# Optimization experiments

Measured on AMD Instinct MI355X. Metric: run time of the kernel, lower is better.

The kernel has to match this reference:

```python
import jax, jax.numpy as jnp
import numpy as np

# Dimensions
B_, T_, IN_ = 8, 1024, 512          # batch, seq_len, in_dim
D_ = 1024                           # latent_dim (hidden_size)
I_ = 2048                           # intermediate_size
N_ = 64                             # state_size
H_ = 16                             # ssm_num_head
P_ = I_ // H_                       # head_dim = 128
K_ = 3                              # conv_kernel
L_ = 4                              # num_layer
OUT_, CB_ = 512, 1024               # out_dim, num_code_book
CONV_DIM = I_ + 2 * N_              # 2176
PROJ = I_ + CONV_DIM + H_           # in_proj width of mixer = 4240


def setup_inputs() -> dict:
    key = jax.random.key(0)
    ks = jax.random.split(key, 16)
    s = 0.02
    inp = {
        "x": jax.random.normal(ks[0], (B_, T_, IN_), jnp.float32),
        "in_w": jax.random.normal(ks[1], (IN_, D_), jnp.float32) * s,
        "in_b": jnp.zeros((D_,), jnp.float32),
        "norm_w": jnp.ones((L_, D_), jnp.float32),
        "mix_in_w": jax.random.normal(ks[2], (L_, D_, PROJ), jnp.float32) * s,
        "conv_w": jax.random.normal(ks[3], (L_, K_, 1, CONV_DIM), jnp.float32) * s,
        "conv_b": jnp.zeros((L_, CONV_DIM), jnp.float32),
        "dt_bias": jax.random.normal(ks[4], (L_, H_), jnp.float32) * 0.1,
        "A_log": jnp.log(jax.random.uniform(ks[5], (L_, H_), jnp.float32, 0.001, 0.1)),
        "D": jnp.ones((L_, H_), jnp.float32),
        "gnorm_w": jnp.ones((L_, I_), jnp.float32),
        "mix_out_w": jax.random.normal(ks[6], (L_, I_, D_), jnp.float32) * s,
        "out_w": jax.random.normal(ks[7], (D_, OUT_), jnp.float32) * s,
        "out_b": jnp.zeros((OUT_,), jnp.float32),
        "code_w": jax.random.normal(ks[8], (D_, CB_), jnp.float32) * s,
        "code_b": jnp.zeros((CB_,), jnp.float32),
    }
    return inp


def rmsnorm(x, w, eps=1e-6):
    v = jnp.mean(jnp.square(x), axis=-1, keepdims=True)
    return x * jax.lax.rsqrt(v + eps) * w


def mamba_block(x, nw, inw, cw, cb, dtb, alog, Dv, gnw, outw):
    residual = x
    h = rmsnorm(x, nw)
    proj = h @ inw                                   # [B,T,PROJ]
    gate, hBC, dt = jnp.split(proj, [I_, I_ + CONV_DIM], axis=-1)
    # causal depthwise conv along time
    conv = jax.lax.conv_general_dilated(
        hBC, cw, window_strides=(1,), padding=[(K_ - 1, 0)],
        dimension_numbers=("NWC", "WIO", "NWC"), feature_group_count=CONV_DIM)
    conv = jax.nn.silu(conv + cb)
    xs, Bm, Cm = jnp.split(conv, [I_, I_ + N_], axis=-1)   # [B,T,I],[B,T,N],[B,T,N]
    dt = jax.nn.softplus(dt + dtb)                   # [B,T,H]
    a = -jnp.exp(alog)                               # [H] scalar decay per head
    xh = xs.reshape(B_, T_, H_, P_)

    def step(hst, inp):
        dt_t, B_t, C_t, x_t = inp                    # [B,H],[B,N],[B,N],[B,H,P]
        dA = jnp.exp(dt_t * a)                       # [B,H]
        hst = hst * dA[:, :, None, None] + (dt_t[:, :, None, None] * x_t[..., None]) * B_t[:, None, None, :]
        y = jnp.einsum("bhpn,bn->bhp", hst, C_t)
        return hst, y

    inputs = (dt.transpose(1, 0, 2), Bm.transpose(1, 0, 2),
              Cm.transpose(1, 0, 2), xh.transpose(1, 0, 2, 3))
    h0 = jnp.zeros((B_, H_, P_, N_), x.dtype)
    _, ys = jax.lax.scan(step, h0, inputs)           # ys: [T,B,H,P]
    y = ys.transpose(1, 0, 2, 3) + Dv[None, None, :, None] * xh
    y = y.reshape(B_, T_, I_)
    y = rmsnorm(y * jax.nn.silu(gate), gnw)          # gated RMSNorm
    return residual + y @ outw


def reference(x, in_w, in_b, norm_w, mix_in_w, conv_w, conv_b, dt_bias,
              A_log, D, gnorm_w, mix_out_w, out_w, out_b, code_w, code_b):
    h = x @ in_w + in_b
    for i in range(L_):
        h = mamba_block(h, norm_w[i], mix_in_w[i], conv_w[i], conv_b[i],
                        dt_bias[i], A_log[i], D[i], gnorm_w[i], mix_out_w[i])
    return (h @ out_w + out_b, h @ code_w + code_b)
```

## Files before the change

### kernel.cpp

```cpp
#include <hip/hip_runtime.h>
#include <hip/hip_bf16.h>

typedef __hip_bfloat16 bf16;
typedef __bf16 bfv8 __attribute__((ext_vector_type(8)));
typedef float fv4 __attribute__((ext_vector_type(4)));

#define B_  8
#define T_  1024
#define INP 512
#define D_  1024
#define I_  2048
#define N_  64
#define H_  16
#define P_  128
#define L_  4
#define OUT_ 512
#define CB_ 1024
#define CONV_DIM 2176
#define PROJ 4240
#define M_  (B_*T_)
#define TC  64
#define NC  (T_/TC)

typedef const __attribute__((address_space(1))) void gv_t;
typedef __attribute__((address_space(3))) void lv_t;

__device__ __forceinline__ void load_lds16(const bf16* g, char* l) {
    __builtin_amdgcn_global_load_lds((gv_t*)g, (lv_t*)l, 16, 0, 0);
}

template <int N> __device__ __forceinline__ void wait_vm() {
    if constexpr (N == 0)      asm volatile("s_waitcnt vmcnt(0)" ::: "memory");
    else if constexpr (N == 2) asm volatile("s_waitcnt vmcnt(2)" ::: "memory");
    else if constexpr (N == 3) asm volatile("s_waitcnt vmcnt(3)" ::: "memory");
    else if constexpr (N == 4) asm volatile("s_waitcnt vmcnt(4)" ::: "memory");
    else if constexpr (N == 6) asm volatile("s_waitcnt vmcnt(6)" ::: "memory");
    else                       asm volatile("s_waitcnt vmcnt(8)" ::: "memory");
}
__device__ __forceinline__ void barrier_sync() {
    asm volatile("s_barrier" ::: "memory");
}

__device__ __forceinline__ fv4 MF(bfv8 a, bfv8 b, fv4 c) {
    return __builtin_amdgcn_mfma_f32_16x16x32_bf16(a, b, c, 0, 0, 0);
}
__device__ __forceinline__ __bf16 f2b(float x) {
    __hip_bfloat16 h = __float2bfloat16(x);
    union { unsigned short u; __bf16 b; } t;
    t.u = *reinterpret_cast<unsigned short*>(&h);
    return t.b;
}
__device__ __forceinline__ float bb2f(__bf16 x) {
    union { __bf16 b; unsigned short u; } t; t.b = x;
    union { unsigned int u; float f; } r; r.u = (unsigned int)t.u << 16;
    return r.f;
}
__device__ __forceinline__ bfv8 cvt8f(const float* p) {
    float4 a = *(const float4*)p, b = *(const float4*)(p + 4);
    bfv8 r;
    r[0] = f2b(a.x); r[1] = f2b(a.y); r[2] = f2b(a.z); r[3] = f2b(a.w);
    r[4] = f2b(b.x); r[5] = f2b(b.y); r[6] = f2b(b.z); r[7] = f2b(b.w);
    return r;
}

__global__ __launch_bounds__(256) void ingest_k(const float* __restrict__ src,
                                                bf16* __restrict__ dst, int n) {
    int i = blockIdx.x * 256 + threadIdx.x;
    if (i >= n) return;
    dst[i] = __float2bfloat16(src[i]);
}

__global__ __launch_bounds__(256) void transpose_any(const float* __restrict__ in,
                                                     size_t off,
                                                     bf16* __restrict__ out,
                                                     int R, int C) {
    __shared__ bf16 tile[32][33];
    int c0 = blockIdx.x * 32, r0 = blockIdx.y * 32;
    int tx = threadIdx.x, ty = threadIdx.y;
#pragma unroll
    for (int i = 0; i < 4; ++i) {
        int r = r0 + ty + i * 8, c = c0 + tx;
        bf16 v = __float2bfloat16(0.f);
        if (c < C) v = __float2bfloat16(in[off + (size_t)r * C + c]);
        tile[ty + i * 8][tx] = v;
    }
    __syncthreads();
#pragma unroll
    for (int i = 0; i < 4; ++i) {
        int c = c0 + ty + i * 8;
        out[(size_t)c * R + r0 + tx] = tile[tx][ty + i * 8];
    }
}

template <int MODE, int BM, int BN, int WGM, int WGN, int RING, int NTHR>
__global__ __launch_bounds__(NTHR) void gemm8p(const bf16* __restrict__ A,
                                               const bf16* __restrict__ Bt,
                                               int K, int N,
                                               const bf16* __restrict__ bias,
                                               float* __restrict__ outF,
                                               bf16* __restrict__ outB,
                                               bf16* __restrict__ outB2,
                                               float* __restrict__ outF2) {
    constexpr int HK = 32;
    constexpr int MT = BM / WGM / 16;
    constexpr int NT = BN / WGN / 16;
    constexpr int ABY = BM * HK * 2;
    constexpr int BBY = BN * HK * 2;
    constexpr int BUF = ABY + BBY;
    constexpr int RPI = NTHR / 4;
    constexpr int AL = BM / RPI;
    constexpr int BL = BN / RPI;
    constexpr int LD = AL + BL;
    constexpr int IB = NTHR * 16;

    extern __shared__ char lds[];
    const int tid = threadIdx.x;
    const int wv = tid >> 6, lane = tid & 63;
    const int l16 = lane & 15, quad = lane >> 4;
    const int wm = (wv / WGN) * (BM / WGM);
    const int wn = (wv % WGN) * (BN / WGN);

    const int NX = gridDim.x;
    const int nwg = NX * gridDim.y;
    const int orig = blockIdx.y * NX + blockIdx.x;
    const int q = nwg >> 3, r = nwg & 7, xcd = orig & 7, lid = orig >> 3;
    const int wg = (xcd < r ? xcd * (q + 1) : r * (q + 1) + (xcd - r) * q) + lid;
    const int m0 = (wg / NX) * BM;
    const int n0 = (wg % NX) * BN;

    const int srow = tid >> 2, sslot = tid & 3;
    const int swz = (sslot ^ ((srow >> 1) & 3)) << 3;
    const bf16* ga = A  + (size_t)(m0 + srow) * K + swz;
    const bf16* gb = Bt + (size_t)(n0 + srow) * K + swz;
    char* lw = lds + wv * 1024;

    const int HT = K / HK;

    auto stageA = [&](int stg, int rbuf) {
#pragma unroll
        for (int j = 0; j < AL; ++j)
            load_lds16(ga + (size_t)stg * HK + (size_t)(j * RPI) * K,
                       lw + rbuf * BUF + j * IB);
    };
    auto stageB = [&](int stg, int rbuf) {
#pragma unroll
        for (int j = 0; j < BL; ++j)
            load_lds16(gb + (size_t)stg * HK + (size_t)(j * RPI) * K,
                       lw + rbuf * BUF + ABY + j * IB);
    };

#pragma unroll
    for (int h = 0; h < RING - 1; ++h) { stageA(h, h); stageB(h, h); }
    wait_vm<LD>();
    barrier_sync();

    fv4 acc[MT][NT] = {};
    int rb = 0;
    for (int ht = 0; ht < HT; ++ht) {
        const char* Ab = lds + rb * BUF;
        const char* Bb = Ab + ABY;
        const int stg = ht + RING - 1;
        const int sb = (rb == 0) ? RING - 1 : rb - 1;
        const bool dostage = stg < HT;

        bfv8 bf[NT], af[MT];
#pragma unroll
        for (int i = 0; i < NT; ++i) {
            int rr = wn + i * 16 + l16;
            bf[i] = *(const bfv8*)(Bb + rr * 64 + ((quad ^ ((rr >> 1) & 3)) << 4));
        }
#pragma unroll
        for (int i = 0; i < MT; ++i) {
            int rr = wm + i * 16 + l16;
            af[i] = *(const bfv8*)(Ab + rr * 64 + ((quad ^ ((rr >> 1) & 3)) << 4));
        }
        if (dostage) { stageA(stg, sb); stageB(stg, sb); }
        __builtin_amdgcn_s_setprio(1);
#pragma unroll
        for (int mt = 0; mt < MT; ++mt)
#pragma unroll
            for (int nt = 0; nt < NT; ++nt)
                acc[mt][nt] = MF(af[mt], bf[nt], acc[mt][nt]);
        __builtin_amdgcn_s_setprio(0);

        int fut = HT - 1 - ht; if (fut > RING - 1) fut = RING - 1;
        if (fut >= 1) {
            int w = (fut - 1) * LD;
            if (w >= LD) wait_vm<LD>();
            else wait_vm<0>();
        }
        barrier_sync();
        rb = (rb + 1 == RING) ? 0 : rb + 1;
    }

#pragma unroll
    for (int mt = 0; mt < MT; ++mt) {
#pragma unroll
        for (int nt = 0; nt < NT; ++nt) {
#pragma unroll
            for (int i = 0; i < 4; ++i) {
                int row = m0 + wm + mt * 16 + quad * 4 + i;
                int col = n0 + wn + nt * 16 + l16;
                float v = acc[mt][nt][i];
                if (MODE == 0) {
                    v += __bfloat162float(bias[col]);
                    outF[(size_t)row * N + col] = v;
                } else if (MODE == 1) {
                    if (col < I_)
                        outB[(size_t)row * I_ + col] = __float2bfloat16(v);
                    else if (col < I_ + CONV_DIM)
                        outB2[(size_t)row * CONV_DIM + (col - I_)] = __float2bfloat16(v);
                    else if (col < PROJ)
                        outF2[(size_t)row * H_ + (col - (I_ + CONV_DIM))] = v;
                } else if (MODE == 2) {
                    outF[(size_t)row * N + col] += v;
                }
            }
        }
    }
}

__global__ __launch_bounds__(256) void rmsnorm_k(const float* __restrict__ x,
                                                 const bf16* __restrict__ w,
                                                 bf16* __restrict__ out) {
    int row = blockIdx.x, tid = threadIdx.x;
    float4 v = *(const float4*)&x[(size_t)row * D_ + tid * 4];
    float ss = v.x * v.x + v.y * v.y + v.z * v.z + v.w * v.w;
#pragma unroll
    for (int off = 32; off; off >>= 1) ss += __shfl_down(ss, off);
    __shared__ float sb[4];
    if ((tid & 63) == 0) sb[tid >> 6] = ss;
    __syncthreads();
    ss = sb[0] + sb[1] + sb[2] + sb[3];
    float rs = rsqrtf(ss * (1.f / D_) + 1e-6f);
    float xv[4] = {v.x, v.y, v.z, v.w};
#pragma unroll
    for (int j = 0; j < 4; ++j)
        out[(size_t)row * D_ + tid * 4 + j] =
            __float2bfloat16(xv[j] * rs * __bfloat162float(w[tid * 4 + j]));
}

__global__ __launch_bounds__(256) void gatednorm_k(const bf16* __restrict__ y,
                                                   const bf16* __restrict__ g,
                                                   const bf16* __restrict__ w,
                                                   bf16* __restrict__ out) {
    int row = blockIdx.x, tid = threadIdx.x;
    size_t base = (size_t)row * I_ + tid * 8;
    bf16 yv[8], gv[8];
    *(uint4*)yv = *(const uint4*)&y[base];
    *(uint4*)gv = *(const uint4*)&g[base];
    float vv[8]; float ss = 0.f;
#pragma unroll
    for (int j = 0; j < 8; ++j) {
        float yf = __bfloat162float(yv[j]);
        float gf = __bfloat162float(gv[j]);
        float sig = 1.f / (1.f + expf(-gf));
        vv[j] = yf * gf * sig;
        ss += vv[j] * vv[j];
    }
#pragma unroll
    for (int off = 32; off; off >>= 1) ss += __shfl_down(ss, off);
    __shared__ float sb[4];
    if ((tid & 63) == 0) sb[tid >> 6] = ss;
    __syncthreads();
    ss = sb[0] + sb[1] + sb[2] + sb[3];
    float rs = rsqrtf(ss * (1.f / I_) + 1e-6f);
    bf16 ov[8];
#pragma unroll
    for (int j = 0; j < 8; ++j)
        ov[j] = __float2bfloat16(vv[j] * rs * __bfloat162float(w[tid * 8 + j]));
    *(uint4*)&out[base] = *(uint4*)ov;
}

__global__ __launch_bounds__(256) void conv_k(const bf16* __restrict__ hbc,
                                              const bf16* __restrict__ w,
                                              const bf16* __restrict__ bias,
                                              bf16* __restrict__ xs,
                                              float* __restrict__ bc) {
    int cq = blockIdx.x * 256 + threadIdx.x;
    if (cq >= CONV_DIM / 4) return;
    int c = cq * 4;
    int bt = blockIdx.y;
    int t = bt & (T_ - 1);
    float acc[4];
#pragma unroll
    for (int j = 0; j < 4; ++j) acc[j] = __bfloat162float(bias[c + j]);
#pragma unroll
    for (int k = 0; k < 3; ++k) {
        int tt = t - 2 + k;
        if (tt < 0) continue;
        const bf16* src = &hbc[(size_t)(bt - 2 + k) * CONV_DIM + c];
#pragma unroll
        for (int j = 0; j < 4; ++j)
            acc[j] = fmaf(__bfloat162float(w[k * CONV_DIM + c + j]),
                          __bfloat162float(src[j]), acc[j]);
    }
#pragma unroll
    for (int j = 0; j < 4; ++j) {
        float v = acc[j];
        v = v / (1.f + expf(-v));
        if (c + j < I_) xs[(size_t)bt * I_ + c + j] = __float2bfloat16(v);
        else            bc[(size_t)bt * 128 + (c + j - I_)] = v;
    }
}

__global__ __launch_bounds__(256) void dtprep_k(const float* __restrict__ dtraw,
                                                const float* __restrict__ dtb,
                                                const float* __restrict__ alog,
                                                float* __restrict__ wco,
                                                float* __restrict__ gma) {
    int chain = blockIdx.x * 4 + (threadIdx.x >> 6);
    int s = threadIdx.x & 63;
    int h = chain & 15, ci = (chain >> 4) & (NC - 1), b = chain >> 8;
    float a = -expf(alog[h]);
    float bz = dtb[h];
    int idx = (b * T_ + ci * TC + s) * H_ + h;
    float z = dtraw[idx] + bz;
    float dt = fmaxf(z, 0.f) + log1pf(expf(-fabsf(z)));
    float ps = dt * a;
#pragma unroll
    for (int d = 1; d < 64; d <<= 1) {
        float o = __shfl_up(ps, d, 64);
        if (s >= d) ps += o;
    }
    float g = expf(ps);
    wco[idx] = dt / g;
    gma[idx] = g;
}

__global__ __launch_bounds__(256) void xpose_k(const bf16* __restrict__ in,
                                               bf16* __restrict__ out) {
    __shared__ bf16 tl[64][72];
    int t0 = blockIdx.x * 64;
    int by = blockIdx.y;
    int pg = by & 1, h = (by >> 1) & 15, b = by >> 5;
    int p0 = pg * 64;
    int tx = threadIdx.x & 15, ty = threadIdx.x >> 4;
#pragma unroll
    for (int i = 0; i < 4; ++i) {
        ushort4 v = *(const ushort4*)&in[(size_t)(b * T_ + t0 + ty + 16 * i) * 2048
                                         + h * 128 + p0 + tx * 4];
        tl[ty + 16 * i][tx * 4 + 0] = *(bf16*)&v.x;
        tl[ty + 16 * i][tx * 4 + 1] = *(bf16*)&v.y;
        tl[ty + 16 * i][tx * 4 + 2] = *(bf16*)&v.z;
        tl[ty + 16 * i][tx * 4 + 3] = *(bf16*)&v.w;
    }
    __syncthreads();
#pragma unroll
    for (int i = 0; i < 4; ++i) {
        ushort4 v;
        v.x = *(unsigned short*)&tl[tx * 4 + 0][ty + 16 * i];
        v.y = *(unsigned short*)&tl[tx * 4 + 1][ty + 16 * i];
        v.z = *(unsigned short*)&tl[tx * 4 + 2][ty + 16 * i];
        v.w = *(unsigned short*)&tl[tx * 4 + 3][ty + 16 * i];
        *(ushort4*)&out[(size_t)((b * 16 + h) * 128 + p0 + ty + 16 * i) * 1024
                        + t0 + tx * 4] = v;
    }
}

__global__ __launch_bounds__(256) void btpose_k(const float* __restrict__ in,
                                                bf16* __restrict__ out) {
    __shared__ bf16 tl[64][72];
    int t0 = blockIdx.x * 64;
    int b = blockIdx.y;
    int tx = threadIdx.x & 15, ty = threadIdx.x >> 4;
#pragma unroll
    for (int i = 0; i < 4; ++i) {
        float4 v = *(const float4*)&in[(size_t)(b * T_ + t0 + ty + 16 * i) * 128 + tx * 4];
        tl[ty + 16 * i][tx * 4 + 0] = __float2bfloat16(v.x);
        tl[ty + 16 * i][tx * 4 + 1] = __float2bfloat16(v.y);
        tl[ty + 16 * i][tx * 4 + 2] = __float2bfloat16(v.z);
        tl[ty + 16 * i][tx * 4 + 3] = __float2bfloat16(v.w);
    }
    __syncthreads();
#pragma unroll
    for (int i = 0; i < 4; ++i) {
        ushort4 v;
        v.x = *(unsigned short*)&tl[tx * 4 + 0][ty + 16 * i];
        v.y = *(unsigned short*)&tl[tx * 4 + 1][ty + 16 * i];
        v.z = *(unsigned short*)&tl[tx * 4 + 2][ty + 16 * i];
        v.w = *(unsigned short*)&tl[tx * 4 + 3][ty + 16 * i];
        *(ushort4*)&out[(size_t)(b * 64 + ty + 16 * i) * 1024 + t0 + tx * 4] = v;
    }
}

__global__ __launch_bounds__(256) void scan_mm_k(const float* __restrict__ bc,
                                                 const bf16* __restrict__ xt,
                                                 const bf16* __restrict__ btb,
                                                 const float* __restrict__ wco,
                                                 const float* __restrict__ gma,
                                                 const float* __restrict__ dvec,
                                                 const bf16* __restrict__ xs,
                                                 bf16* __restrict__ yout,
                                                 bf16* __restrict__ sfin) {
    __shared__ __align__(64) char plds[4][8192];
    const int wv = threadIdx.x >> 6, lane = threadIdx.x & 63;
    const int l16 = lane & 15, quad = lane >> 4;
    const int wid = blockIdx.x * 4 + wv;
    const int ci = wid & (NC - 1), h = (wid >> 4) & (H_ - 1), b = wid >> 8;
    const int bt0 = b * T_ + ci * TC;
    char* Pb = plds[wv];

    float wl = wco[(size_t)(bt0 + lane) * H_ + h];
    float gl = gma[(size_t)(bt0 + lane) * H_ + h];
    float g63 = __shfl(gl, 63);
    float Dv = dvec[h];

    float wsv[4], gmv[4][4];
#pragma unroll
    for (int s4 = 0; s4 < 4; ++s4) wsv[s4] = __shfl(wl, s4 * 16 + l16);
#pragma unroll
    for (int t4 = 0; t4 < 4; ++t4)
#pragma unroll
        for (int i = 0; i < 4; ++i) gmv[t4][i] = __shfl(gl, t4 * 16 + quad * 4 + i);

    fv4 g[4][4] = {};
#pragma unroll
    for (int kq = 0; kq < 2; ++kq) {
        bfv8 cf[4], bfr[4];
#pragma unroll
        for (int i = 0; i < 4; ++i) {
            cf[i]  = cvt8f(&bc[(size_t)(bt0 + i * 16 + l16) * 128 + 64 + kq * 32 + quad * 8]);
            bfr[i] = cvt8f(&bc[(size_t)(bt0 + i * 16 + l16) * 128 + kq * 32 + quad * 8]);
        }
#pragma unroll
        for (int t4 = 0; t4 < 4; ++t4)
#pragma unroll
            for (int s4 = 0; s4 < 4; ++s4)
                g[t4][s4] = MF(cf[t4], bfr[s4], g[t4][s4]);
    }

#pragma unroll
    for (int t4 = 0; t4 < 4; ++t4)
#pragma unroll
        for (int s4 = 0; s4 < 4; ++s4)
#pragma unroll
            for (int i = 0; i < 4; ++i) {
                int t = t4 * 16 + quad * 4 + i, s = s4 * 16 + l16;
                float pv = (s <= t) ? g[t4][s4][i] * gmv[t4][i] * wsv[s4] : 0.f;
                int slot = (s >> 3) ^ (t & 7);
                *(__bf16*)(Pb + t * 128 + slot * 16 + (s & 7) * 2) = f2b(pv);
            }

    bfv8 xf[8][2];
    const bf16* xtp = xt + (size_t)((b * 16 + h) * 128) * 1024 + ci * 64;
#pragma unroll
    for (int p4 = 0; p4 < 8; ++p4)
#pragma unroll
        for (int kq = 0; kq < 2; ++kq)
            xf[p4][kq] = *(const bfv8*)&xtp[(size_t)(p4 * 16 + l16) * 1024 + kq * 32 + quad * 8];

    fv4 y[4][8] = {};
#pragma unroll
    for (int t4 = 0; t4 < 4; ++t4) {
#pragma unroll
        for (int kq = 0; kq < ((t4 < 2) ? 1 : 2); ++kq) {
            int rr = t4 * 16 + l16;
            bfv8 pf = *(const bfv8*)(Pb + rr * 128 + (((kq * 4 + quad) ^ (rr & 7)) << 4));
#pragma unroll
            for (int p4 = 0; p4 < 8; ++p4)
                y[t4][p4] = MF(pf, xf[p4][kq], y[t4][p4]);
        }
    }

    bf16* yp = yout + (size_t)bt0 * I_ + h * P_;
    const bf16* xp = xs + (size_t)bt0 * I_ + h * P_;
#pragma unroll
    for (int t4 = 0; t4 < 4; ++t4)
#pragma unroll
        for (int p4 = 0; p4 < 8; ++p4)
#pragma unroll
            for (int i = 0; i < 4; ++i) {
                size_t a = (size_t)(t4 * 16 + quad * 4 + i) * I_ + p4 * 16 + l16;
                float xv = __bfloat162float(xp[a]);
                yp[a] = __float2bfloat16(y[t4][p4][i] + Dv * xv);
            }

    float ws8[2][8];
#pragma unroll
    for (int kq = 0; kq < 2; ++kq)
#pragma unroll
        for (int j = 0; j < 8; ++j)
            ws8[kq][j] = g63 * __shfl(wl, kq * 32 + quad * 8 + j);

    fv4 sa[8][4] = {};
    const bf16* btp = btb + (size_t)b * 64 * 1024 + ci * 64;
#pragma unroll
    for (int kq = 0; kq < 2; ++kq) {
        bfv8 sbv[4];
#pragma unroll
        for (int n4 = 0; n4 < 4; ++n4) {
            bfv8 raw = *(const bfv8*)&btp[(size_t)(n4 * 16 + l16) * 1024 + kq * 32 + quad * 8];
            bfv8 sb;
#pragma unroll
            for (int j = 0; j < 8; ++j) sb[j] = f2b(bb2f(raw[j]) * ws8[kq][j]);
            sbv[n4] = sb;
        }
#pragma unroll
        for (int p4 = 0; p4 < 8; ++p4)
#pragma unroll
            for (int n4 = 0; n4 < 4; ++n4)
                sa[p4][n4] = MF(xf[p4][kq], sbv[n4], sa[p4][n4]);
    }

    bf16* sp = sfin + (size_t)wid * (128 * 64);
#pragma unroll
    for (int p4 = 0; p4 < 8; ++p4)
#pragma unroll
        for (int n4 = 0; n4 < 4; ++n4)
#pragma unroll
            for (int i = 0; i < 4; ++i)
                sp[(p4 * 16 + quad * 4 + i) * 64 + n4 * 16 + l16] =
                    __float2bfloat16(sa[p4][n4][i]);
}

__global__ __launch_bounds__(128) void scan_combine_k(bf16* __restrict__ sbuf,
                                                      const float* __restrict__ gma) {
    int bid = blockIdx.x;
    int n = bid & 63;
    int h = (bid >> 6) & (H_ - 1);
    int b = bid >> 10;
    int p = threadIdx.x;
    size_t base0 = ((size_t)(b * (H_ * NC) + h * NC) * (128 * 64)) + n * 128 + p;
    int gbase = b * T_ * H_ + h;
    float S = 0.f;
#pragma unroll
    for (int ci = 0; ci < NC; ++ci) {
        bf16* addr = sbuf + base0 + (size_t)ci * (128 * 64);
        float tmp = __bfloat162float(*addr);
        *addr = __float2bfloat16(S);
        float G = gma[gbase + (ci * TC + TC - 1) * H_];
        S = fmaf(G, S, tmp);
    }
}

__global__ __launch_bounds__(256) void scan_corr_k(const float* __restrict__ bc,
                                                   const bf16* __restrict__ sfin,
                                                   const float* __restrict__ gma,
                                                   bf16* __restrict__ yout) {
    const int wv = threadIdx.x >> 6, lane = threadIdx.x & 63;
    const int wid = blockIdx.x * 4 + wv;
    const int ci = wid & (NC - 1), h = (wid >> 4) & (H_ - 1), b = wid >> 8;
    if (ci == 0) return;
    const int l16 = lane & 15, quad = lane >> 4;
    const int bt0 = b * T_ + ci * TC;

    float gl = gma[(size_t)(bt0 + lane) * H_ + h];
    float gmv[4][4];
#pragma unroll
    for (int t4 = 0; t4 < 4; ++t4)
#pragma unroll
        for (int i = 0; i < 4; ++i) gmv[t4][i] = __shfl(gl, t4 * 16 + quad * 4 + i);

    const bf16* sp = sfin + (size_t)wid * (128 * 64);
    fv4 z[4][8] = {};
#pragma unroll
    for (int kq = 0; kq < 2; ++kq) {
        bfv8 cf[4];
#pragma unroll
        for (int i = 0; i < 4; ++i)
            cf[i] = cvt8f(&bc[(size_t)(bt0 + i * 16 + l16) * 128 + 64 + kq * 32 + quad * 8]);
#pragma unroll
        for (int p4 = 0; p4 < 8; ++p4) {
            bfv8 sf = *(const bfv8*)&sp[(p4 * 16 + l16) * 64 + kq * 32 + quad * 8];
#pragma unroll
            for (int t4 = 0; t4 < 4; ++t4)
                z[t4][p4] = MF(cf[t4], sf, z[t4][p4]);
        }
    }

    bf16* yp = yout + (size_t)bt0 * I_ + h * P_;
#pragma unroll
    for (int t4 = 0; t4 < 4; ++t4)
#pragma unroll
        for (int i = 0; i < 4; ++i) {
            float gm = gmv[t4][i];
#pragma unroll
            for (int p4 = 0; p4 < 8; ++p4) {
                size_t a = (size_t)(t4 * 16 + quad * 4 + i) * I_ + p4 * 16 + l16;
                float yv = __bfloat162float(yp[a]);
                yp[a] = __float2bfloat16(yv + gm * z[t4][p4][i]);
            }
        }
}

__global__ __launch_bounds__(256) void cast_f2b_k(const float* __restrict__ in,
                                                  bf16* __restrict__ out) {
    int i = (blockIdx.x * 256 + threadIdx.x) * 4;
    float4 v = *(const float4*)&in[i];
    bf16 ov[4] = {__float2bfloat16(v.x), __float2bfloat16(v.y),
                  __float2bfloat16(v.z), __float2bfloat16(v.w)};
    *(uint2*)&out[i] = *(uint2*)ov;
}


static inline size_t align256(size_t x) { return (x + 255) & ~(size_t)255; }

extern "C" void kernel_launch(void* const* d_in, const int* in_sizes, int n_in,
                              void* d_out, int out_size, void* d_ws, size_t ws_size,
                              hipStream_t stream) {
    const float* x_in     = (const float*)d_in[0];
    const float* in_w     = (const float*)d_in[1];
    const float* in_b     = (const float*)d_in[2];
    const float* norm_w   = (const float*)d_in[3];
    const float* mix_in_w = (const float*)d_in[4];
    const float* conv_w   = (const float*)d_in[5];
    const float* conv_b   = (const float*)d_in[6];
    const float* dt_bias  = (const float*)d_in[7];
    const float* A_log    = (const float*)d_in[8];
    const float* Dvec     = (const float*)d_in[9];
    const float* gnorm_w  = (const float*)d_in[10];
    const float* mix_out_w= (const float*)d_in[11];
    const float* out_w    = (const float*)d_in[12];
    const float* out_b    = (const float*)d_in[13];
    const float* code_w   = (const float*)d_in[14];
    const float* code_b   = (const float*)d_in[15];
    float* outF0 = (float*)d_out;
    float* outF1 = (float*)d_out + (size_t)M_ * OUT_;

    char* p = (char*)d_ws;
    auto alloc = [&](size_t bytes) -> char* { char* r = p; p += align256(bytes); return r; };

    bf16*  xt       = (bf16*)alloc((size_t)B_ * H_ * 128 * T_ * 2);
    bf16*  hn       = xt;
    bf16*  xb       = xt + (size_t)M_ * D_;
    bf16*  v_inb    = (bf16*)alloc(D_ * 2);
    bf16*  v_normw  = (bf16*)alloc(L_ * D_ * 2);
    bf16*  v_convw  = (bf16*)alloc(L_ * 3 * CONV_DIM * 2);
    bf16*  v_convb  = (bf16*)alloc(L_ * CONV_DIM * 2);
    bf16*  v_gnw    = (bf16*)alloc(L_ * I_ * 2);
    bf16*  v_outb   = (bf16*)alloc(OUT_ * 2);
    bf16*  v_codeb  = (bf16*)alloc(CB_ * 2);
    bf16*  wt_in    = (bf16*)alloc((size_t)1024 * 512 * 2);
    bf16*  wt_big   = (bf16*)alloc((size_t)4352 * 1024 * 2);
    bf16*  wt_small = (bf16*)alloc((size_t)1024 * 2048 * 2);
    bf16*  wt_out   = (bf16*)alloc((size_t)512 * 1024 * 2);
    bf16*  wt_code  = (bf16*)alloc((size_t)1024 * 1024 * 2);
    float* hbuf     = (float*)alloc((size_t)M_ * D_ * 4);
    bf16*  gate     = (bf16*)alloc((size_t)M_ * I_ * 2);
    bf16*  hbc      = (bf16*)alloc((size_t)M_ * CONV_DIM * 2);
    float* dtraw    = (float*)alloc((size_t)M_ * H_ * 4);
    bf16*  xs       = (bf16*)alloc((size_t)M_ * I_ * 2);
    float* bcbuf    = (float*)alloc((size_t)M_ * 128 * 4);
    float* wcob     = (float*)alloc((size_t)M_ * H_ * 4);
    float* gmab     = (float*)alloc((size_t)M_ * H_ * 4);
    bf16*  sfin     = (bf16*)alloc((size_t)B_ * H_ * NC * 128 * 64 * 2);
    bf16*  bt16     = (bf16*)alloc((size_t)B_ * 64 * T_ * 2);
    (void)in_sizes; (void)n_in; (void)out_size;

    size_t needed = (size_t)(p - (char*)d_ws);
    if (needed > ws_size) return;

    constexpr size_t SH_PROJ = 73728;
    constexpr size_t SH_SQ   = 49152;
    static bool attr_done = false;
    if (!attr_done) {
        attr_done = true;
        (void)hipFuncSetAttribute((const void*)gemm8p<1, 256, 128, 4, 2, 3, 512>,
                                  hipFuncAttributeMaxDynamicSharedMemorySize, (int)SH_PROJ);
        (void)hipFuncSetAttribute((const void*)gemm8p<0, 128, 128, 2, 2, 3, 256>,
                                  hipFuncAttributeMaxDynamicSharedMemorySize, (int)SH_SQ);
        (void)hipFuncSetAttribute((const void*)gemm8p<2, 128, 128, 2, 2, 3, 256>,
                                  hipFuncAttributeMaxDynamicSharedMemorySize, (int)SH_SQ);
    }

    auto ing = [&](const float* src, bf16* dst, int n) {
        ingest_k<<<(n + 255) / 256, 256, 0, stream>>>(src, dst, n);
    };
    ing(x_in, xb, M_ * INP);
    ing(in_b, v_inb, D_);
    ing(norm_w, v_normw, L_ * D_);
    ing(conv_w, v_convw, L_ * 3 * CONV_DIM);
    ing(conv_b, v_convb, L_ * CONV_DIM);
    ing(gnorm_w, v_gnw, L_ * I_);
    ing(out_b, v_outb, OUT_);
    ing(code_b, v_codeb, CB_);

    dim3 tb(32, 8);
    transpose_any<<<dim3(32, 16), tb, 0, stream>>>(in_w, 0, wt_in, 512, 1024);
    transpose_any<<<dim3(16, 32), tb, 0, stream>>>(out_w, 0, wt_out, 1024, 512);
    transpose_any<<<dim3(32, 32), tb, 0, stream>>>(code_w, 0, wt_code, 1024, 1024);

    gemm8p<0, 128, 128, 2, 2, 3, 256><<<dim3(8, 64), 256, SH_SQ, stream>>>(
        xb, wt_in, INP, D_, v_inb, hbuf, nullptr, nullptr, nullptr);

    for (int i = 0; i < L_; ++i) {
        transpose_any<<<dim3(136, 32), tb, 0, stream>>>(mix_in_w, (size_t)i * 1024 * PROJ,
                                                        wt_big, 1024, PROJ);
        transpose_any<<<dim3(32, 64), tb, 0, stream>>>(mix_out_w, (size_t)i * 2048 * 1024,
                                                       wt_small, 2048, 1024);
        rmsnorm_k<<<M_, 256, 0, stream>>>(hbuf, v_normw + i * D_, hn);
        gemm8p<1, 256, 128, 4, 2, 3, 512><<<dim3(34, 32), 512, SH_PROJ, stream>>>(
            hn, wt_big, D_, 4352, nullptr, nullptr, gate, hbc, dtraw);
        conv_k<<<dim3(3, M_), 256, 0, stream>>>(hbc, v_convw + i * 3 * CONV_DIM,
                                                v_convb + i * CONV_DIM, xs, bcbuf);
        dtprep_k<<<B_ * NC * H_ / 4, 256, 0, stream>>>(
            dtraw, dt_bias + i * H_, A_log + i * H_, wcob, gmab);
        xpose_k<<<dim3(16, 256), 256, 0, stream>>>(xs, xt);
        btpose_k<<<dim3(16, 8), 256, 0, stream>>>(bcbuf, bt16);
        scan_mm_k<<<512, 256, 0, stream>>>(bcbuf, xt, bt16, wcob, gmab,
                                           Dvec + i * H_, xs, hbc, sfin);
        scan_combine_k<<<B_ * H_ * 64, 128, 0, stream>>>(sfin, gmab);
        scan_corr_k<<<512, 256, 0, stream>>>(bcbuf, sfin, gmab, hbc);
        gatednorm_k<<<M_, 256, 0, stream>>>(hbc, gate, v_gnw + i * I_, xs);
        gemm8p<2, 128, 128, 2, 2, 3, 256><<<dim3(8, 64), 256, SH_SQ, stream>>>(
            xs, wt_small, I_, D_, nullptr, hbuf, nullptr, nullptr, nullptr);
    }

    cast_f2b_k<<<(M_ * D_) / 1024, 256, 0, stream>>>(hbuf, hn);
    gemm8p<0, 128, 128, 2, 2, 3, 256><<<dim3(4, 64), 256, SH_SQ, stream>>>(
        hn, wt_out, D_, OUT_, v_outb, outF0, nullptr, nullptr, nullptr);
    gemm8p<0, 128, 128, 2, 2, 3, 256><<<dim3(8, 64), 256, SH_SQ, stream>>>(
        hn, wt_code, D_, CB_, v_codeb, outF1, nullptr, nullptr, nullptr);
}
```

Measured before the change: 1.647 ms.

## Fuse output heads GEMM, retile in_proj GEMM, vectorize conv, shrink scan registers

Merges the two final head GEMMs into a single GEMM over a concatenated weight with a new epilogue mode that splits columns between the two outputs, saving one launch and one read of the activations. Retiles the large in_proj GEMM from 256x128 tiles with 512 threads to 128x128 tiles with 256 threads, doubling the grid. Vectorizes the conv kernel's loads and stores, and restructures the scan kernel so the y accumulator lives per time-tile instead of for all four at once, lowering register pressure. The smaller GEMM tile may reduce data reuse.

```diff
diff --git a/kernel.cpp b/kernel.cpp
--- a/kernel.cpp
+++ b/kernel.cpp
@@ -214,6 +214,10 @@
                         outF2[(size_t)row * H_ + (col - (I_ + CONV_DIM))] = v;
                 } else if (MODE == 2) {
                     outF[(size_t)row * N + col] += v;
+                } else if (MODE == 3) {
+                    v += __bfloat162float(bias[col]);
+                    if (col < OUT_) outF[(size_t)row * OUT_ + col] = v;
+                    else            outF2[(size_t)row * CB_ + (col - OUT_)] = v;
                 }
             }
         }
@@ -282,25 +286,30 @@
     int c = cq * 4;
     int bt = blockIdx.y;
     int t = bt & (T_ - 1);
+    bf16 bv[4]; *(uint2*)bv = *(const uint2*)&bias[c];
     float acc[4];
 #pragma unroll
-    for (int j = 0; j < 4; ++j) acc[j] = __bfloat162float(bias[c + j]);
+    for (int j = 0; j < 4; ++j) acc[j] = __bfloat162float(bv[j]);
 #pragma unroll
     for (int k = 0; k < 3; ++k) {
-        int tt = t - 2 + k;
-        if (tt < 0) continue;
-        const bf16* src = &hbc[(size_t)(bt - 2 + k) * CONV_DIM + c];
+        if (t - 2 + k < 0) continue;
+        bf16 wv[4], sv[4];
+        *(uint2*)wv = *(const uint2*)&w[k * CONV_DIM + c];
+        *(uint2*)sv = *(const uint2*)&hbc[(size_t)(bt - 2 + k) * CONV_DIM + c];
 #pragma unroll
         for (int j = 0; j < 4; ++j)
-            acc[j] = fmaf(__bfloat162float(w[k * CONV_DIM + c + j]),
-                          __bfloat162float(src[j]), acc[j]);
-    }
-#pragma unroll
-    for (int j = 0; j < 4; ++j) {
-        float v = acc[j];
-        v = v / (1.f + expf(-v));
-        if (c + j < I_) xs[(size_t)bt * I_ + c + j] = __float2bfloat16(v);
-        else            bc[(size_t)bt * 128 + (c + j - I_)] = v;
+            acc[j] = fmaf(__bfloat162float(wv[j]), __bfloat162float(sv[j]), acc[j]);
+    }
+#pragma unroll
+    for (int j = 0; j < 4; ++j) acc[j] = acc[j] / (1.f + expf(-acc[j]));
+    if (c < I_) {
+        bf16 ov[4];
+#pragma unroll
+        for (int j = 0; j < 4; ++j) ov[j] = __float2bfloat16(acc[j]);
+        *(uint2*)&xs[(size_t)bt * I_ + c] = *(uint2*)ov;
+    } else {
+        float4 o; o.x = acc[0]; o.y = acc[1]; o.z = acc[2]; o.w = acc[3];
+        *(float4*)&bc[(size_t)bt * 128 + (c - I_)] = o;
     }
 }
 
@@ -450,31 +459,28 @@
         for (int kq = 0; kq < 2; ++kq)
             xf[p4][kq] = *(const bfv8*)&xtp[(size_t)(p4 * 16 + l16) * 1024 + kq * 32 + quad * 8];
 
-    fv4 y[4][8] = {};
+    bf16* yp = yout + (size_t)bt0 * I_ + h * P_;
+    const bf16* xp = xs + (size_t)bt0 * I_ + h * P_;
 #pragma unroll
     for (int t4 = 0; t4 < 4; ++t4) {
+        fv4 y[8] = {};
 #pragma unroll
         for (int kq = 0; kq < ((t4 < 2) ? 1 : 2); ++kq) {
             int rr = t4 * 16 + l16;
             bfv8 pf = *(const bfv8*)(Pb + rr * 128 + (((kq * 4 + quad) ^ (rr & 7)) << 4));
 #pragma unroll
             for (int p4 = 0; p4 < 8; ++p4)
-                y[t4][p4] = MF(pf, xf[p4][kq], y[t4][p4]);
-        }
-    }
-
-    bf16* yp = yout + (size_t)bt0 * I_ + h * P_;
-    const bf16* xp = xs + (size_t)bt0 * I_ + h * P_;
-#pragma unroll
-    for (int t4 = 0; t4 < 4; ++t4)
+                y[p4] = MF(pf, xf[p4][kq], y[p4]);
+        }
 #pragma unroll
         for (int p4 = 0; p4 < 8; ++p4)
 #pragma unroll
             for (int i = 0; i < 4; ++i) {
                 size_t a = (size_t)(t4 * 16 + quad * 4 + i) * I_ + p4 * 16 + l16;
                 float xv = __bfloat162float(xp[a]);
-                yp[a] = __float2bfloat16(y[t4][p4][i] + Dv * xv);
+                yp[a] = __float2bfloat16(y[p4][i] + Dv * xv);
             }
+    }
 
     float ws8[2][8];
 #pragma unroll
@@ -629,13 +635,11 @@
     bf16*  v_convw  = (bf16*)alloc(L_ * 3 * CONV_DIM * 2);
     bf16*  v_convb  = (bf16*)alloc(L_ * CONV_DIM * 2);
     bf16*  v_gnw    = (bf16*)alloc(L_ * I_ * 2);
-    bf16*  v_outb   = (bf16*)alloc(OUT_ * 2);
-    bf16*  v_codeb  = (bf16*)alloc(CB_ * 2);
+    bf16*  v_headb  = (bf16*)alloc((OUT_ + CB_) * 2);
     bf16*  wt_in    = (bf16*)alloc((size_t)1024 * 512 * 2);
     bf16*  wt_big   = (bf16*)alloc((size_t)4352 * 1024 * 2);
     bf16*  wt_small = (bf16*)alloc((size_t)1024 * 2048 * 2);
-    bf16*  wt_out   = (bf16*)alloc((size_t)512 * 1024 * 2);
-    bf16*  wt_code  = (bf16*)alloc((size_t)1024 * 1024 * 2);
+    bf16*  wt_head  = (bf16*)alloc((size_t)1536 * 1024 * 2);
     float* hbuf     = (float*)alloc((size_t)M_ * D_ * 4);
     bf16*  gate     = (bf16*)alloc((size_t)M_ * I_ * 2);
     bf16*  hbc      = (bf16*)alloc((size_t)M_ * CONV_DIM * 2);
@@ -651,16 +655,17 @@
     size_t needed = (size_t)(p - (char*)d_ws);
     if (needed > ws_size) return;
 
-    constexpr size_t SH_PROJ = 73728;
-    constexpr size_t SH_SQ   = 49152;
+    constexpr size_t SH_SQ = 49152;
     static bool attr_done = false;
     if (!attr_done) {
         attr_done = true;
-        (void)hipFuncSetAttribute((const void*)gemm8p<1, 256, 128, 4, 2, 3, 512>,
-                                  hipFuncAttributeMaxDynamicSharedMemorySize, (int)SH_PROJ);
         (void)hipFuncSetAttribute((const void*)gemm8p<0, 128, 128, 2, 2, 3, 256>,
                                   hipFuncAttributeMaxDynamicSharedMemorySize, (int)SH_SQ);
+        (void)hipFuncSetAttribute((const void*)gemm8p<1, 128, 128, 2, 2, 3, 256>,
+                                  hipFuncAttributeMaxDynamicSharedMemorySize, (int)SH_SQ);
         (void)hipFuncSetAttribute((const void*)gemm8p<2, 128, 128, 2, 2, 3, 256>,
+                                  hipFuncAttributeMaxDynamicSharedMemorySize, (int)SH_SQ);
+        (void)hipFuncSetAttribute((const void*)gemm8p<3, 128, 128, 2, 2, 3, 256>,
                                   hipFuncAttributeMaxDynamicSharedMemorySize, (int)SH_SQ);
     }
 
@@ -673,13 +678,14 @@
     ing(conv_w, v_convw, L_ * 3 * CONV_DIM);
     ing(conv_b, v_convb, L_ * CONV_DIM);
     ing(gnorm_w, v_gnw, L_ * I_);
-    ing(out_b, v_outb, OUT_);
-    ing(code_b, v_codeb, CB_);
+    ing(out_b, v_headb, OUT_);
+    ing(code_b, v_headb + OUT_, CB_);
 
     dim3 tb(32, 8);
     transpose_any<<<dim3(32, 16), tb, 0, stream>>>(in_w, 0, wt_in, 512, 1024);
-    transpose_any<<<dim3(16, 32), tb, 0, stream>>>(out_w, 0, wt_out, 1024, 512);
-    transpose_any<<<dim3(32, 32), tb, 0, stream>>>(code_w, 0, wt_code, 1024, 1024);
+    transpose_any<<<dim3(16, 32), tb, 0, stream>>>(out_w, 0, wt_head, 1024, 512);
+    transpose_any<<<dim3(32, 32), tb, 0, stream>>>(code_w, 0, wt_head + (size_t)512 * 1024,
+                                                   1024, 1024);
 
     gemm8p<0, 128, 128, 2, 2, 3, 256><<<dim3(8, 64), 256, SH_SQ, stream>>>(
         xb, wt_in, INP, D_, v_inb, hbuf, nullptr, nullptr, nullptr);
@@ -690,7 +696,7 @@
         transpose_any<<<dim3(32, 64), tb, 0, stream>>>(mix_out_w, (size_t)i * 2048 * 1024,
                                                        wt_small, 2048, 1024);
         rmsnorm_k<<<M_, 256, 0, stream>>>(hbuf, v_normw + i * D_, hn);
-        gemm8p<1, 256, 128, 4, 2, 3, 512><<<dim3(34, 32), 512, SH_PROJ, stream>>>(
+        gemm8p<1, 128, 128, 2, 2, 3, 256><<<dim3(34, 64), 256, SH_SQ, stream>>>(
             hn, wt_big, D_, 4352, nullptr, nullptr, gate, hbc, dtraw);
         conv_k<<<dim3(3, M_), 256, 0, stream>>>(hbc, v_convw + i * 3 * CONV_DIM,
                                                 v_convb + i * CONV_DIM, xs, bcbuf);
@@ -708,8 +714,6 @@
     }
 
     cast_f2b_k<<<(M_ * D_) / 1024, 256, 0, stream>>>(hbuf, hn);
-    gemm8p<0, 128, 128, 2, 2, 3, 256><<<dim3(4, 64), 256, SH_SQ, stream>>>(
-        hn, wt_out, D_, OUT_, v_outb, outF0, nullptr, nullptr, nullptr);
-    gemm8p<0, 128, 128, 2, 2, 3, 256><<<dim3(8, 64), 256, SH_SQ, stream>>>(
-        hn, wt_code, D_, CB_, v_codeb, outF1, nullptr, nullptr, nullptr);
-}
+    gemm8p<3, 128, 128, 2, 2, 3, 256><<<dim3(12, 64), 256, SH_SQ, stream>>>(
+        hn, wt_head, D_, 1536, v_headb, outF0, nullptr, nullptr, outF1);
+}
```

Measured after the change: 1.624 ms. No clear change (-1.4%).
